# Optimization experiments

Hardware: AMD Instinct MI355X
Metric: run time of the kernel (lower is better)

The kernel has to match this reference:

```python
import jax, jax.numpy as jnp
import numpy as np

BN_EPS = 1e-5


def conv(x, w, b=None, stride=1, pad=1):
    out = jax.lax.conv_general_dilated(
        x, w, (stride, stride), [(pad, pad), (pad, pad)],
        dimension_numbers=("NCHW", "OIHW", "NCHW"))
    if b is not None:
        out = out + b[None, :, None, None]
    return out


def bn_relu(x):
    # BatchNorm2d(affine=False) in training mode: per-channel batch stats
    mean = jnp.mean(x, axis=(0, 2, 3), keepdims=True)
    var = jnp.var(x, axis=(0, 2, 3), keepdims=True)
    return jax.nn.relu((x - mean) * jax.lax.rsqrt(var + BN_EPS))


def deform_conv(x, offset, w, b, stride, pad=1):
    # torchvision DeformConv2d semantics, 3x3 kernel, dilation=1
    B, C, H, W = x.shape
    O = w.shape[0]
    K = 9
    Ho, Wo = offset.shape[2], offset.shape[3]
    off = offset.reshape(B, K, 2, Ho, Wo)  # (dy, dx) per kernel tap
    ky, kx = jnp.meshgrid(jnp.arange(3), jnp.arange(3), indexing="ij")
    ky = ky.reshape(K).astype(x.dtype)
    kx = kx.reshape(K).astype(x.dtype)
    oy = (jnp.arange(Ho) * stride - pad).astype(x.dtype)
    ox = (jnp.arange(Wo) * stride - pad).astype(x.dtype)
    # sampling coords [B,K,Ho,Wo]
    ys = oy[None, None, :, None] + ky[None, :, None, None] + off[:, :, 0]
    xs = ox[None, None, None, :] + kx[None, :, None, None] + off[:, :, 1]
    y0 = jnp.floor(ys)
    x0 = jnp.floor(xs)
    wy1 = ys - y0
    wx1 = xs - x0
    imf = x.reshape(B, C, H * W)

    def gather(iy, ix):
        valid = (iy >= 0) & (iy <= H - 1) & (ix >= 0) & (ix <= W - 1)
        iyc = jnp.clip(iy, 0, H - 1).astype(jnp.int32)
        ixc = jnp.clip(ix, 0, W - 1).astype(jnp.int32)
        lin = iyc * W + ixc  # [B,K,Ho,Wo]
        g = jax.vmap(lambda im, li: im[:, li])(imf, lin)  # [B,C,K,Ho,Wo]
        return g * valid[:, None].astype(x.dtype)

    sampled = (gather(y0, x0) * ((1 - wy1) * (1 - wx1))[:, None]
               + gather(y0, x0 + 1) * ((1 - wy1) * wx1)[:, None]
               + gather(y0 + 1, x0) * (wy1 * (1 - wx1))[:, None]
               + gather(y0 + 1, x0 + 1) * (wy1 * wx1)[:, None])
    out = jnp.einsum("ock,bckhw->bohw", w.reshape(O, C, K), sampled)
    return out + b[None, :, None, None]


def avgpool4(x):
    B, C, H, W = x.shape
    return x.reshape(B, C, H // 4, 4, W // 4, 4).mean(axis=(3, 5))


def setup_inputs() -> dict:
    key = jax.random.key(0)
    ks = jax.random.split(key, 20)
    n = jax.random.normal
    s = 0.05
    return {
        "x": n(ks[0], (8, 3, 640, 640), jnp.float32),
        "w_off1": n(ks[1], (18, 3, 3, 3), jnp.float32) * s,
        "b_off1": jnp.zeros((18,), jnp.float32),
        "w_d1": n(ks[2], (64, 3, 3, 3), jnp.float32) * s,
        "b_d1": jnp.zeros((64,), jnp.float32),
        "w_skip": n(ks[3], (64, 3, 1, 1), jnp.float32) * s,
        "b_skip": jnp.zeros((64,), jnp.float32),
        "w_bl1": n(ks[4], (64, 64, 3, 3), jnp.float32) * s,
        "w_bl2": n(ks[5], (64, 64, 3, 3), jnp.float32) * s,
        "w_off2": n(ks[6], (18, 64, 3, 3), jnp.float32) * s,
        "b_off2": jnp.zeros((18,), jnp.float32),
        "w_d2": n(ks[7], (64, 64, 3, 3), jnp.float32) * s,
        "b_d2": jnp.zeros((64,), jnp.float32),
        "w_off3": n(ks[8], (18, 64, 3, 3), jnp.float32) * s,
        "b_off3": jnp.zeros((18,), jnp.float32),
        "w_d3": n(ks[9], (256, 64, 3, 3), jnp.float32) * s,
        "b_d3": jnp.zeros((256,), jnp.float32),
    }


def reference(x, w_off1, b_off1, w_d1, b_d1, w_skip, b_skip, w_bl1, w_bl2,
              w_off2, b_off2, w_d2, b_d2, w_off3, b_off3, w_d3, b_d3):
    offset1 = conv(x, w_off1, b_off1, stride=4)
    d1 = deform_conv(x, offset1, w_d1, b_d1, stride=4)
    skip = conv(avgpool4(x), w_skip, b_skip, stride=1, pad=0)
    f = bn_relu(conv(d1 + skip, w_bl1))
    feat_1_4 = bn_relu(conv(f, w_bl2))
    offset2 = conv(feat_1_4, w_off2, b_off2, stride=2)
    feat_1_8 = deform_conv(feat_1_4, offset2, w_d2, b_d2, stride=2)
    offset3 = conv(feat_1_8, w_off3, b_off3, stride=2)
    feat_1_16 = deform_conv(feat_1_8, offset3, w_d3, b_d3, stride=2)
    return (feat_1_4, feat_1_8, feat_1_16)
```

## Files before the change

### kernel.cpp

```cpp
#include <hip/hip_runtime.h>
#include <hip/hip_bf16.h>
#include <math.h>

#define TPB 256

typedef __attribute__((ext_vector_type(8))) short bf16x8_t;
typedef __attribute__((ext_vector_type(4))) float f32x4_t;
typedef __attribute__((ext_vector_type(4))) int i32x4_t;
typedef __attribute__((ext_vector_type(4))) unsigned short u16x4_t;

static __device__ __forceinline__ float bf16_to_f(unsigned short s) {
    union { unsigned u; float f; } cv;
    cv.u = ((unsigned)s) << 16;
    return cv.f;
}
static __device__ __forceinline__ short f_to_bf16(float v) {
    __hip_bfloat16 h = __float2bfloat16(v);
    return *(short*)&h;
}

__global__ void repack_frag_kernel(const float* __restrict__ w,
                                   short* __restrict__ wtf,
                                   int Oreal, int NFRAG)
{
    int idx = blockIdx.x * TPB + threadIdx.x;
    int total = 18 * NFRAG * 64 * 8;
    if (idx >= total) return;
    int j    = idx & 7;
    int lane = (idx >> 3) & 63;
    int t    = idx >> 9;
    int ocf  = t % NFRAG;
    int kc   = t / NFRAG;
    int oc   = ocf * 16 + (lane & 15);
    int tap  = kc >> 1;
    int ic   = (kc & 1) * 32 + (lane >> 4) * 8 + j;
    float v = 0.f;
    if (oc < Oreal)
        v = w[((size_t)(oc * 64 + ic)) * 9 + tap];
    wtf[idx] = f_to_bf16(v);
}

__global__ void repack_d1_kernel(const float* __restrict__ w,
                                 short* __restrict__ wtf)
{
    int idx = blockIdx.x * TPB + threadIdx.x;
    if (idx >= 2048) return;
    int j    = idx & 7;
    int lane = (idx >> 3) & 63;
    int ocf  = idx >> 9;
    int oc   = ocf * 16 + (lane & 15);
    int k    = (lane >> 4) * 8 + j;
    float v = 0.f;
    if (k < 27) v = w[(size_t)oc * 27 + k];
    wtf[idx] = f_to_bf16(v);
}

template <int NORM>
__global__ __launch_bounds__(256, 2) void conv3x3_mfma_kernel(
    const short* __restrict__ xh,
    const short* __restrict__ wt,
    short* __restrict__ outh,
    float* __restrict__ stats,
    const float* __restrict__ stats_in,
    float invN,
    const float* __restrict__ zp)
{
    __shared__ short tile[2816 * 8];
    __shared__ float sstat[128];
    __shared__ float sm[64], sr[64];
    const int H = 160, W = 160, HW = 25600;
    int blk = blockIdx.x;
    int b  = blk / 100;
    int r  = blk % 100;
    int y0 = (r / 10) * 16;
    int x0 = (r % 10) * 16;
    const int tid = threadIdx.x;
    const short* inb = xh + (size_t)b * HW * 64;

    if (tid < 128) sstat[tid] = 0.f;
    if (NORM) {
        if (tid < 64) {
            float s = 0.f, s2 = 0.f;
#pragma unroll
            for (int k = 0; k < 8; ++k) {
                s  += stats_in[k * 128 + tid];
                s2 += stats_in[k * 128 + 64 + tid];
            }
            float mean = s * invN;
            float var  = s2 * invN - mean * mean;
            sm[tid] = mean;
            sr[tid] = rsqrtf(var + 1e-5f);
        }
        __syncthreads();
    }

#pragma unroll
    for (int it = 0; it < 11; ++it) {
        int item = it * 256 + tid;
        int c8  = item & 7;
        int pix = item >> 3;
        int row = pix / 18;
        int col = pix - row * 18;
        int y = y0 + row - 1;
        int x = x0 + col - 1;
        bool ok = (pix < 324) & (y >= 0) & (y < H) & (x >= 0) & (x < W);
        int cs = c8 ^ (col & 7);
        const short* src = ok
            ? &inb[((size_t)y * W + x) * 64 + (cs << 3)]
            : (const short*)zp;
        bf16x8_t v = *(const bf16x8_t*)src;
        if (NORM) {
            int cs8 = cs << 3;
            bf16x8_t o;
#pragma unroll
            for (int j = 0; j < 8; ++j) {
                float f = (bf16_to_f((unsigned short)v[j]) - sm[cs8 + j]) * sr[cs8 + j];
                f = f > 0.f ? f : 0.f;
                o[j] = ok ? f_to_bf16(f) : (short)0;
            }
            v = o;
        }
        *(bf16x8_t*)&tile[item * 8] = v;
    }
    __syncthreads();

    const int wv  = tid >> 6;
    const int l   = tid & 63;
    const int l15 = l & 15;
    const int lg  = l >> 4;

    f32x4_t acc[4][4];
#pragma unroll
    for (int i = 0; i < 4; ++i)
#pragma unroll
        for (int j = 0; j < 4; ++j)
            acc[i][j] = (f32x4_t){0.f, 0.f, 0.f, 0.f};

    bf16x8_t bfp[2][4], afp[2][4];
#pragma unroll
    for (int nf = 0; nf < 4; ++nf)
        bfp[0][nf] = *(const bf16x8_t*)(wt + (((size_t)(0 * 4 + nf)) * 64 + l) * 8);
    {
        int colr = l15;
        int chunk = lg ^ (colr & 7);
#pragma unroll
        for (int mf = 0; mf < 4; ++mf)
            afp[0][mf] = *(const bf16x8_t*)&tile[((wv * 4 + mf) * 18 + colr) * 64 + chunk * 8];
    }
#pragma unroll
    for (int kc = 0; kc < 18; ++kc) {
        const int cur = kc & 1, nxt = cur ^ 1;
        if (kc + 1 < 18) {
            int kn = kc + 1;
#pragma unroll
            for (int nf = 0; nf < 4; ++nf)
                bfp[nxt][nf] = *(const bf16x8_t*)(wt + (((size_t)(kn * 4 + nf)) * 64 + l) * 8);
            int tap = kn >> 1;
            int dy = tap / 3, dx = tap % 3;
            int colr = l15 + dx;
            int chunk = (((kn & 1) << 2) + lg) ^ (colr & 7);
#pragma unroll
            for (int mf = 0; mf < 4; ++mf)
                afp[nxt][mf] = *(const bf16x8_t*)&tile[((wv * 4 + mf + dy) * 18 + colr) * 64 + chunk * 8];
        }
#pragma unroll
        for (int mf = 0; mf < 4; ++mf)
#pragma unroll
            for (int nf = 0; nf < 4; ++nf)
                acc[mf][nf] = __builtin_amdgcn_mfma_f32_16x16x32_bf16(
                    afp[cur][mf], bfp[cur][nf], acc[mf][nf], 0, 0, 0);
    }

    __syncthreads();
#pragma unroll
    for (int mf = 0; mf < 4; ++mf) {
        int py = wv * 4 + mf;
#pragma unroll
        for (int nf = 0; nf < 4; ++nf) {
            int oc = nf * 16 + l15;
#pragma unroll
            for (int k = 0; k < 4; ++k)
                tile[((py * 16) + lg * 4 + k) * 64 + oc] = f_to_bf16(acc[mf][nf][k]);
        }
    }
    __syncthreads();
    short* outb = outh + (size_t)b * HW * 64;
#pragma unroll
    for (int j = 0; j < 8; ++j) {
        int item = j * 256 + tid;
        int c8  = item & 7;
        int pix = item >> 3;
        int py  = pix >> 4, px = pix & 15;
        *(bf16x8_t*)&outb[((size_t)(y0 + py) * W + x0 + px) * 64 + c8 * 8] =
            *(bf16x8_t*)&tile[pix * 64 + c8 * 8];
    }

#pragma unroll
    for (int nf = 0; nf < 4; ++nf) {
        float s = 0.f, s2 = 0.f;
#pragma unroll
        for (int mf = 0; mf < 4; ++mf)
#pragma unroll
            for (int k = 0; k < 4; ++k) {
                float v = acc[mf][nf][k];
                s += v; s2 += v * v;
            }
        s  += __shfl_xor(s, 16, 64);  s  += __shfl_xor(s, 32, 64);
        s2 += __shfl_xor(s2, 16, 64); s2 += __shfl_xor(s2, 32, 64);
        if (lg == 0) {
            int oc = nf * 16 + l15;
            atomicAdd(&sstat[oc], s);
            atomicAdd(&sstat[64 + oc], s2);
        }
    }
    __syncthreads();
    float* st = stats + (size_t)(blockIdx.x & 7) * 128;
    if (tid < 128) atomicAdd(&st[tid], sstat[tid]);
}

__global__ void nchw_to_nhwc_bf16_kernel(const float* __restrict__ in,
                                         short* __restrict__ out, int HW)
{
    __shared__ short tile[64][66];
    int nchunks = HW >> 6;
    int b  = blockIdx.x / nchunks;
    int p0 = (blockIdx.x % nchunks) << 6;
    int tid = threadIdx.x;
#pragma unroll
    for (int rep = 0; rep < 16; ++rep) {
        int item = rep * 256 + tid;
        int c = item >> 6, p = item & 63;
        tile[p][c] = f_to_bf16(in[((size_t)b * 64 + c) * HW + p0 + p]);
    }
    __syncthreads();
#pragma unroll
    for (int rep = 0; rep < 16; ++rep) {
        int item = rep * 256 + tid;
        int p = item >> 6, c = item & 63;
        out[((size_t)b * HW + p0 + p) * 64 + c] = tile[p][c];
    }
}

__global__ void bn_apply_dual_kernel(const short* __restrict__ in,
                                     const float* __restrict__ stats,
                                     float* __restrict__ out,
                                     short* __restrict__ outh,
                                     int HW, float invN)
{
    __shared__ float ftile[64][65];
    __shared__ float sm[64], sr[64];
    int nchunks = HW >> 6;
    int b  = blockIdx.x / nchunks;
    int p0 = (blockIdx.x % nchunks) << 6;
    int tid = threadIdx.x;
    if (tid < 64) {
        float s = 0.f, s2 = 0.f;
#pragma unroll
        for (int k = 0; k < 8; ++k) {
            s  += stats[k * 128 + tid];
            s2 += stats[k * 128 + 64 + tid];
        }
        float mean = s * invN;
        float var  = s2 * invN - mean * mean;
        sm[tid] = mean;
        sr[tid] = rsqrtf(var + 1e-5f);
    }
    __syncthreads();
#pragma unroll
    for (int it = 0; it < 2; ++it) {
        int item = it * 256 + tid;
        int p = item >> 3, c0 = (item & 7) * 8;
        size_t gi = ((size_t)(b * HW + p0 + p)) * 64 + c0;
        bf16x8_t v = *(const bf16x8_t*)&in[gi];
        bf16x8_t o;
#pragma unroll
        for (int j = 0; j < 8; ++j) {
            float f = (bf16_to_f((unsigned short)v[j]) - sm[c0 + j]) * sr[c0 + j];
            f = f > 0.f ? f : 0.f;
            ftile[p][c0 + j] = f;
            o[j] = f_to_bf16(f);
        }
        *(bf16x8_t*)&outh[gi] = o;
    }
    __syncthreads();
#pragma unroll
    for (int rep = 0; rep < 16; ++rep) {
        int item = rep * 256 + tid;
        int c = item >> 6, p = item & 63;
        out[((size_t)b * 64 + c) * HW + p0 + p] = ftile[p][c];
    }
}

__global__ void x_to_nhwc4_kernel(const float* __restrict__ in,
                                  float* __restrict__ out)
{
    int idx = blockIdx.x * TPB + threadIdx.x;
    const int HW = 640 * 640;
    if (idx >= 8 * HW) return;
    int b = idx / HW, p = idx % HW;
    f32x4_t v;
    v[0] = in[((size_t)b * 3 + 0) * HW + p];
    v[1] = in[((size_t)b * 3 + 1) * HW + p];
    v[2] = in[((size_t)b * 3 + 2) * HW + p];
    v[3] = 0.f;
    *(f32x4_t*)&out[(size_t)idx * 4] = v;
}

__global__ __launch_bounds__(256, 1) void offconv_mfma_kernel(
    const short* __restrict__ xh,
    const short* __restrict__ wt,
    const float* __restrict__ bias,
    float* __restrict__ out,
    int H, int W, int Ho, int Wo)
{
    const int HW = Ho * Wo;
    const int tid = threadIdx.x;
    const int wv = tid >> 6, l = tid & 63;
    const int l15 = l & 15, lg = l >> 4;
    const int pix0 = blockIdx.x * 64 + wv * 16;
    const int b = pix0 / HW;
    const int r0 = pix0 - b * HW;

    int rp = r0 + l15;
    int ho = rp / Wo, wo = rp % Wo;
    const short* xb = xh + (size_t)b * H * W * 64;

    f32x4_t acc[2];
    acc[0] = (f32x4_t){0.f, 0.f, 0.f, 0.f};
    acc[1] = (f32x4_t){0.f, 0.f, 0.f, 0.f};

#pragma unroll 2
    for (int kc = 0; kc < 18; ++kc) {
        int tap = kc >> 1;
        int iy = ho * 2 - 1 + tap / 3;
        int ix = wo * 2 - 1 + tap % 3;
        bf16x8_t af = {};
        if (iy >= 0 && iy < H && ix >= 0 && ix < W)
            af = *(const bf16x8_t*)&xb[((size_t)iy * W + ix) * 64
                                       + (kc & 1) * 32 + lg * 8];
#pragma unroll
        for (int nf = 0; nf < 2; ++nf) {
            bf16x8_t bf = *(const bf16x8_t*)(wt + (((size_t)(kc * 2 + nf)) * 64 + l) * 8);
            acc[nf] = __builtin_amdgcn_mfma_f32_16x16x32_bf16(af, bf, acc[nf], 0, 0, 0);
        }
    }

#pragma unroll
    for (int nf = 0; nf < 2; ++nf) {
        int oc = nf * 16 + l15;
        if (oc < 18) {
            float bv = bias[oc];
            f32x4_t v = acc[nf];
            v[0] += bv; v[1] += bv; v[2] += bv; v[3] += bv;
            *(f32x4_t*)&out[((size_t)(b * 18 + oc)) * HW + r0 + lg * 4] = v;
        }
    }
}

__global__ __launch_bounds__(256, 1) void deform1_kernel(
    const float* __restrict__ x4,
    const float* __restrict__ wof,
    const float* __restrict__ bof,
    const short* __restrict__ wtd1,
    const float* __restrict__ bias,
    const float* __restrict__ pool,
    const float* __restrict__ wsk,
    const float* __restrict__ bsk,
    short* __restrict__ outh)
{
    const int H = 640, W = 640, Ho = 160, Wo = 160, HW = 25600;
    constexpr int P = 32;
    __shared__ float xtap[P * 9][4];
    __shared__ float swof[486];
    __shared__ float sbof[18];
    __shared__ float spool[3][P];
    __shared__ float off1[P][18];
    __shared__ alignas(16) short sampb[P][40];
    __shared__ int   sidx[P * 9][4];
    __shared__ float swt[P * 9][4];
    const int tid = threadIdx.x;
    const int pix0 = blockIdx.x * P;
    const int b = pix0 / HW;
    const int r0 = pix0 - b * HW;
    const float* xb = x4 + (size_t)b * H * W * 4;

    for (int item = tid; item < P * 9; item += TPB) {
        int p = item / 9, tap = item % 9;
        int r = r0 + p, ho = r / Wo, wo = r % Wo;
        int iy = ho * 4 - 1 + tap / 3;
        int ix = wo * 4 - 1 + tap % 3;
        f32x4_t s = (f32x4_t){0.f, 0.f, 0.f, 0.f};
        if (iy >= 0 && iy < H && ix >= 0 && ix < W)
            s = *(const f32x4_t*)&xb[((size_t)iy * W + ix) * 4];
        *(f32x4_t*)xtap[item] = s;
    }
    for (int i = tid; i < P * 40; i += TPB) ((short*)sampb)[i] = 0;
    for (int i = tid; i < 96; i += TPB) {
        int c = i >> 5, p = i & 31;
        spool[c][p] = pool[((size_t)(b * 3 + c)) * HW + r0 + p];
    }
    for (int item = tid; item < 486; item += TPB) swof[item] = wof[item];
    if (tid < 18) sbof[tid] = bof[tid];
    __syncthreads();

    for (int item = tid; item < P * 18; item += TPB) {
        int p = item / 18, o = item % 18;
        float acc = sbof[o];
#pragma unroll
        for (int tap = 0; tap < 9; ++tap) {
            const float* xt = xtap[p * 9 + tap];
#pragma unroll
            for (int c = 0; c < 3; ++c)
                acc += xt[c] * swof[(o * 3 + c) * 9 + tap];
        }
        off1[p][o] = acc;
    }
    __syncthreads();

    for (int item = tid; item < P * 9; item += TPB) {
        int p = item / 9, tap = item % 9;
        int r = r0 + p, ho = r / Wo, wo = r % Wo;
        float dy = off1[p][2 * tap];
        float dx = off1[p][2 * tap + 1];
        float ys = (float)(ho * 4 - 1 + tap / 3) + dy;
        float xs = (float)(wo * 4 - 1 + tap % 3) + dx;
        float y0f = floorf(ys), x0f = floorf(xs);
        float fy = ys - y0f, fx = xs - x0f;
        int y0 = (int)y0f, x0 = (int)x0f;
        float wts[4] = {(1.f - fy) * (1.f - fx), (1.f - fy) * fx,
                        fy * (1.f - fx),          fy * fx};
#pragma unroll
        for (int j = 0; j < 4; ++j) {
            int iy = y0 + (j >> 1), ix = x0 + (j & 1);
            bool v = (iy >= 0) && (iy < H) && (ix >= 0) && (ix < W);
            sidx[item][j] = v ? (iy * W + ix) : 0;
            swt[item][j]  = v ? wts[j] : 0.f;
        }
    }
    __syncthreads();

    for (int item = tid; item < P * 9; item += TPB) {
        int p = item / 9, tap = item % 9;
        i32x4_t id4 = *(const i32x4_t*)sidx[item];
        f32x4_t w4  = *(const f32x4_t*)swt[item];
        f32x4_t a0 = *(const f32x4_t*)&xb[(size_t)(unsigned)id4[0] * 4];
        f32x4_t a1 = *(const f32x4_t*)&xb[(size_t)(unsigned)id4[1] * 4];
        f32x4_t a2 = *(const f32x4_t*)&xb[(size_t)(unsigned)id4[2] * 4];
        f32x4_t a3 = *(const f32x4_t*)&xb[(size_t)(unsigned)id4[3] * 4];
        sampb[p][0 * 9 + tap] = f_to_bf16(
            w4[0]*a0[0] + w4[1]*a1[0] + w4[2]*a2[0] + w4[3]*a3[0]);
        sampb[p][1 * 9 + tap] = f_to_bf16(
            w4[0]*a0[1] + w4[1]*a1[1] + w4[2]*a2[1] + w4[3]*a3[1]);
        sampb[p][2 * 9 + tap] = f_to_bf16(
            w4[0]*a0[2] + w4[1]*a1[2] + w4[2]*a2[2] + w4[3]*a3[2]);
    }
    __syncthreads();

    const int wv = tid >> 6;
    const int l  = tid & 63;
    const int l15 = l & 15, lg = l >> 4;
    bf16x8_t bf  = *(const bf16x8_t*)(wtd1 + (((size_t)wv * 64 + l)) * 8);
    bf16x8_t af0 = *(const bf16x8_t*)&sampb[l15][lg * 8];
    bf16x8_t af1 = *(const bf16x8_t*)&sampb[l15 + 16][lg * 8];
    f32x4_t z = (f32x4_t){0.f, 0.f, 0.f, 0.f};
    f32x4_t acc0 = __builtin_amdgcn_mfma_f32_16x16x32_bf16(af0, bf, z, 0, 0, 0);
    f32x4_t acc1 = __builtin_amdgcn_mfma_f32_16x16x32_bf16(af1, bf, z, 0, 0, 0);

    int oc = wv * 16 + l15;
    float bb = bias[oc] + bsk[oc];
    float w0 = wsk[oc * 3 + 0], w1 = wsk[oc * 3 + 1], w2 = wsk[oc * 3 + 2];
    short* otile = (short*)xtap;
    __syncthreads();
#pragma unroll
    for (int mf = 0; mf < 2; ++mf) {
        f32x4_t a = mf ? acc1 : acc0;
#pragma unroll
        for (int k = 0; k < 4; ++k) {
            int px = mf * 16 + lg * 4 + k;
            float sv = w0 * spool[0][px] + w1 * spool[1][px] + w2 * spool[2][px];
            otile[px * 64 + oc] = f_to_bf16(a[k] + bb + sv);
        }
    }
    __syncthreads();
    {
        int c8 = tid & 7, px = tid >> 3;
        *(bf16x8_t*)&outh[((size_t)(b * HW + r0 + px)) * 64 + c8 * 8] =
            *(bf16x8_t*)&otile[px * 64 + c8 * 8];
    }
}

template <int O>
__global__ __launch_bounds__(256, 1) void deform_mfma_kernel(
    const short* __restrict__ xh,
    const float* __restrict__ off,
    const short* __restrict__ wt,
    const float* __restrict__ bias,
    float* __restrict__ out,
    int H, int W, int Ho, int Wo, int stride)
{
    constexpr int NF = O / 64;
    constexpr int NFRAG = O / 16;
    constexpr int P  = 32;
    __shared__ alignas(16) short samp[P * 576];
    __shared__ int   sidx[P * 9][4];
    __shared__ float swt[P * 9][4];

    const int tid = threadIdx.x;
    const int HW = Ho * Wo;
    const int pix0 = blockIdx.x * P;
    const int b = pix0 / HW;
    const int r0 = pix0 - b * HW;

    for (int item = tid; item < P * 9; item += TPB) {
        int p = item / 9, tap = item % 9;
        int r = r0 + p, ho = r / Wo, wo = r % Wo;
        float dy = off[((size_t)(b * 18 + 2 * tap) * Ho + ho) * Wo + wo];
        float dx = off[((size_t)(b * 18 + 2 * tap + 1) * Ho + ho) * Wo + wo];
        float ys = (float)(ho * stride - 1 + tap / 3) + dy;
        float xs = (float)(wo * stride - 1 + tap % 3) + dx;
        float y0f = floorf(ys), x0f = floorf(xs);
        float fy = ys - y0f, fx = xs - x0f;
        int y0 = (int)y0f, x0 = (int)x0f;
        float wts[4] = {(1.f - fy) * (1.f - fx), (1.f - fy) * fx,
                        fy * (1.f - fx),          fy * fx};
#pragma unroll
        for (int j = 0; j < 4; ++j) {
            int iy = y0 + (j >> 1), ix = x0 + (j & 1);
            bool v = (iy >= 0) && (iy < H) && (ix >= 0) && (ix < W);
            sidx[item][j] = v ? (iy * W + ix) : 0;
            swt[item][j]  = v ? wts[j] : 0.f;
        }
    }
    __syncthreads();

    {
        const int grp = tid >> 4;
        const int ic  = (tid & 15) * 4;
        const short* xb = xh + (size_t)b * H * W * 64;
#pragma unroll 3
        for (int i = 0; i < 18; ++i) {
            int e = grp * 18 + i;
            int p = e / 9, tap = e % 9;
            i32x4_t id4 = *(const i32x4_t*)sidx[e];
            f32x4_t w4  = *(const f32x4_t*)swt[e];
            u16x4_t u0 = *(const u16x4_t*)&xb[(size_t)(unsigned)id4[0] * 64 + ic];
            u16x4_t u1 = *(const u16x4_t*)&xb[(size_t)(unsigned)id4[1] * 64 + ic];
            u16x4_t u2 = *(const u16x4_t*)&xb[(size_t)(unsigned)id4[2] * 64 + ic];
            u16x4_t u3 = *(const u16x4_t*)&xb[(size_t)(unsigned)id4[3] * 64 + ic];
            float v0 = w4[0]*bf16_to_f(u0[0]) + w4[1]*bf16_to_f(u1[0])
                     + w4[2]*bf16_to_f(u2[0]) + w4[3]*bf16_to_f(u3[0]);
            float v1 = w4[0]*bf16_to_f(u0[1]) + w4[1]*bf16_to_f(u1[1])
                     + w4[2]*bf16_to_f(u2[1]) + w4[3]*bf16_to_f(u3[1]);
            float v2 = w4[0]*bf16_to_f(u0[2]) + w4[1]*bf16_to_f(u1[2])
                     + w4[2]*bf16_to_f(u2[2]) + w4[3]*bf16_to_f(u3[2]);
            float v3 = w4[0]*bf16_to_f(u0[3]) + w4[1]*bf16_to_f(u1[3])
                     + w4[2]*bf16_to_f(u2[3]) + w4[3]*bf16_to_f(u3[3]);
            int sw = (tap * 8 + ((ic >> 3) ^ (p & 7))) * 8 + (ic & 7);
            short* dst = &samp[p * 576 + sw];
            dst[0] = f_to_bf16(v0);
            dst[1] = f_to_bf16(v1);
            dst[2] = f_to_bf16(v2);
            dst[3] = f_to_bf16(v3);
        }
    }
    __syncthreads();

    const int wv = tid >> 6;
    const int l  = tid & 63;
    const int l15 = l & 15, lg = l >> 4;
    f32x4_t acc[2][NF];
#pragma unroll
    for (int mf = 0; mf < 2; ++mf)
#pragma unroll
        for (int nf = 0; nf < NF; ++nf)
            acc[mf][nf] = (f32x4_t){0.f, 0.f, 0.f, 0.f};

#pragma unroll 2
    for (int kc = 0; kc < 18; ++kc) {
        int tap = kc >> 1;
        int low = (((kc & 1) << 2) | lg) ^ (l15 & 7);
        bf16x8_t af0 = *(const bf16x8_t*)&samp[l15 * 576 + (tap * 8 + low) * 8];
        bf16x8_t af1 = *(const bf16x8_t*)&samp[(l15 + 16) * 576 + (tap * 8 + low) * 8];
#pragma unroll
        for (int nf = 0; nf < NF; ++nf) {
            int ocf = wv * NF + nf;
            bf16x8_t bf = *(const bf16x8_t*)(wt + (((size_t)(kc * NFRAG + ocf)) * 64 + l) * 8);
            acc[0][nf] = __builtin_amdgcn_mfma_f32_16x16x32_bf16(af0, bf, acc[0][nf], 0, 0, 0);
            acc[1][nf] = __builtin_amdgcn_mfma_f32_16x16x32_bf16(af1, bf, acc[1][nf], 0, 0, 0);
        }
    }

#pragma unroll
    for (int mf = 0; mf < 2; ++mf)
#pragma unroll
        for (int nf = 0; nf < NF; ++nf) {
            int oc = (wv * NF + nf) * 16 + l15;
            float bv = bias[oc];
            f32x4_t v = acc[mf][nf];
            v[0] += bv; v[1] += bv; v[2] += bv; v[3] += bv;
            *(f32x4_t*)&out[((size_t)(b * O + oc)) * HW + r0 + mf * 16 + lg * 4] = v;
        }
}

__global__ void avgpool4_kernel(const float* __restrict__ in,
                                float* __restrict__ out,
                                int BC, int Ho, int Wo, int H, int W)
{
    int idx = blockIdx.x * TPB + threadIdx.x;
    int total = BC * Ho * Wo;
    if (idx >= total) return;
    int wo = idx % Wo;
    int t = idx / Wo;
    int ho = t % Ho;
    int bc = t / Ho;
    const float* xp = in + (size_t)bc * H * W + (ho * 4) * W + wo * 4;
    float s = 0.f;
#pragma unroll
    for (int i = 0; i < 4; ++i)
#pragma unroll
        for (int j = 0; j < 4; ++j)
            s += xp[i * W + j];
    out[idx] = s * (1.0f / 16.0f);
}

__global__ void zero_stats_kernel(float* __restrict__ stats)
{
    int i = threadIdx.x;
#pragma unroll
    for (int k = 0; k < 8; ++k) stats[k * 256 + i] = 0.f;
    stats[2048 + i] = 0.f;
    stats[2048 + 256 + i] = 0.f;
}

extern "C" void kernel_launch(void* const* d_in, const int* in_sizes, int n_in,
                              void* d_out, int out_size, void* d_ws, size_t ws_size,
                              hipStream_t stream)
{
    const float* x      = (const float*)d_in[0];
    const float* w_off1 = (const float*)d_in[1];
    const float* b_off1 = (const float*)d_in[2];
    const float* w_d1   = (const float*)d_in[3];
    const float* b_d1   = (const float*)d_in[4];
    const float* w_skip = (const float*)d_in[5];
    const float* b_skip = (const float*)d_in[6];
    const float* w_bl1  = (const float*)d_in[7];
    const float* w_bl2  = (const float*)d_in[8];
    const float* w_off2 = (const float*)d_in[9];
    const float* b_off2 = (const float*)d_in[10];
    const float* w_d2   = (const float*)d_in[11];
    const float* b_d2   = (const float*)d_in[12];
    const float* w_off3 = (const float*)d_in[13];
    const float* b_off3 = (const float*)d_in[14];
    const float* w_d3   = (const float*)d_in[15];
    const float* b_d3   = (const float*)d_in[16];

    const int B = 8;
    float* A     = (float*)d_ws;
    float* bufB  = A + 3686400;
    float* bufC  = bufB + 13107200;

    short* hB   = (short*)bufB;
    short* hC   = (short*)bufC;
    float* pool = bufB + 8000000;

    short* wt1    = (short*)(A + 1000000);
    short* wt2    = wt1 + 18 * 4 * 512;
    short* wtd2   = (short*)(A + 1500000);
    short* wtd3   = (short*)(A + 1550000);
    short* wtoff2 = (short*)(A + 1700000);
    short* wtoff3 = (short*)(A + 1712000);
    short* wtd1   = (short*)(A + 1750000);
    float* stats1 = A + 1800000;
    float* stats2 = stats1 + 1024;
    float* zpage  = stats1 + 2048;

    float* out0 = (float*)d_out;
    float* out1 = out0 + 13107200;
    float* out2 = out1 + 3276800;

    const float invN = 1.0f / (B * 25600);

    x_to_nhwc4_kernel<<<(8 * 409600 + TPB - 1) / TPB, TPB, 0, stream>>>(x, bufC);

    avgpool4_kernel<<<(B * 3 * 25600 + TPB - 1) / TPB, TPB, 0, stream>>>(
        x, pool, B * 3, 160, 160, 640, 640);

    repack_frag_kernel<<<(18 * 4 * 512 + TPB - 1) / TPB, TPB, 0, stream>>>(w_bl1, wt1, 64, 4);
    repack_frag_kernel<<<(18 * 4 * 512 + TPB - 1) / TPB, TPB, 0, stream>>>(w_bl2, wt2, 64, 4);
    repack_frag_kernel<<<(18 * 4 * 512 + TPB - 1) / TPB, TPB, 0, stream>>>(w_d2, wtd2, 64, 4);
    repack_frag_kernel<<<(18 * 16 * 512 + TPB - 1) / TPB, TPB, 0, stream>>>(w_d3, wtd3, 256, 16);
    repack_frag_kernel<<<(18 * 2 * 512 + TPB - 1) / TPB, TPB, 0, stream>>>(w_off2, wtoff2, 18, 2);
    repack_frag_kernel<<<(18 * 2 * 512 + TPB - 1) / TPB, TPB, 0, stream>>>(w_off3, wtoff3, 18, 2);
    repack_d1_kernel<<<8, TPB, 0, stream>>>(w_d1, wtd1);
    zero_stats_kernel<<<1, 256, 0, stream>>>(stats1);

    deform1_kernel<<<8 * 25600 / 32, TPB, 0, stream>>>(
        bufC, w_off1, b_off1, wtd1, b_d1, pool, w_skip, b_skip, hB);

    conv3x3_mfma_kernel<0><<<800, TPB, 0, stream>>>(
        hB, wt1, hC, stats1, nullptr, invN, zpage);

    conv3x3_mfma_kernel<1><<<800, TPB, 0, stream>>>(
        hC, wt2, hB, stats2, stats1, invN, zpage);

    bn_apply_dual_kernel<<<8 * 400, TPB, 0, stream>>>(
        hB, stats2, out0, hC, 25600, invN);

    offconv_mfma_kernel<<<8 * 6400 / 64, TPB, 0, stream>>>(
        hC, wtoff2, b_off2, A, 160, 160, 80, 80);

    deform_mfma_kernel<64><<<8 * 6400 / 32, TPB, 0, stream>>>(
        hC, A, wtd2, b_d2, out1, 160, 160, 80, 80, 2);

    nchw_to_nhwc_bf16_kernel<<<8 * (6400 / 64), TPB, 0, stream>>>(out1, hB, 6400);

    offconv_mfma_kernel<<<8 * 1600 / 64, TPB, 0, stream>>>(
        hB, wtoff3, b_off3, A, 80, 80, 40, 40);

    deform_mfma_kernel<256><<<8 * 1600 / 32, TPB, 0, stream>>>(
        hB, A, wtd3, b_d3, out2, 80, 80, 40, 40, 2);
}
```

Before: 238.0 us.

## Fuse input prep, weight repacks and NHWC conversion into fewer kernels

Merges the NCHW-to-NHWC4 conversion and the 4x4 average pool into a single prep kernel that reads the input once with vector loads. All weight repacks and the stats zeroing are folded into one launch. The deform conv at 1/8 scale now also writes its bf16 NHWC copy from the accumulators through shared memory, which removes the separate transpose kernel and its re-read of out1. The aim is fewer launches and less global traffic, at the cost of an extra shared-memory pass and sync in the deform kernel.

```diff
diff --git a/kernel.cpp b/kernel.cpp
--- a/kernel.cpp
+++ b/kernel.cpp
@@ -19,13 +19,42 @@
     return *(short*)&h;
 }
 
-__global__ void repack_frag_kernel(const float* __restrict__ w,
-                                   short* __restrict__ wtf,
-                                   int Oreal, int NFRAG)
-{
+__global__ void prep_kernel(const float* __restrict__ in,
+                            float* __restrict__ x4,
+                            float* __restrict__ pool)
+{
+    const int HWo = 25600, H = 640, W = 640;
     int idx = blockIdx.x * TPB + threadIdx.x;
-    int total = 18 * NFRAG * 64 * 8;
-    if (idx >= total) return;
+    if (idx >= 8 * HWo) return;
+    int b = idx / HWo, r = idx % HWo;
+    int ho = r / 160, wo = r % 160;
+    float s0 = 0.f, s1 = 0.f, s2 = 0.f;
+    float* x4b = x4 + (size_t)b * H * W * 4;
+#pragma unroll
+    for (int dy = 0; dy < 4; ++dy) {
+        int row = ho * 4 + dy;
+        size_t base = ((size_t)row * W + wo * 4);
+        f32x4_t a0 = *(const f32x4_t*)&in[((size_t)(b * 3 + 0) * H * W) + base];
+        f32x4_t a1 = *(const f32x4_t*)&in[((size_t)(b * 3 + 1) * H * W) + base];
+        f32x4_t a2 = *(const f32x4_t*)&in[((size_t)(b * 3 + 2) * H * W) + base];
+        s0 += a0[0] + a0[1] + a0[2] + a0[3];
+        s1 += a1[0] + a1[1] + a1[2] + a1[3];
+        s2 += a2[0] + a2[1] + a2[2] + a2[3];
+#pragma unroll
+        for (int dx = 0; dx < 4; ++dx) {
+            f32x4_t v = (f32x4_t){a0[dx], a1[dx], a2[dx], 0.f};
+            *(f32x4_t*)&x4b[(base + dx) * 4] = v;
+        }
+    }
+    pool[((size_t)(b * 3 + 0)) * HWo + r] = s0 * (1.0f / 16.0f);
+    pool[((size_t)(b * 3 + 1)) * HWo + r] = s1 * (1.0f / 16.0f);
+    pool[((size_t)(b * 3 + 2)) * HWo + r] = s2 * (1.0f / 16.0f);
+}
+
+static __device__ __forceinline__ void repack_one(
+    const float* __restrict__ w, short* __restrict__ wtf,
+    int idx, int Oreal, int NFRAG)
+{
     int j    = idx & 7;
     int lane = (idx >> 3) & 63;
     int t    = idx >> 9;
@@ -40,19 +69,40 @@
     wtf[idx] = f_to_bf16(v);
 }
 
-__global__ void repack_d1_kernel(const float* __restrict__ w,
-                                 short* __restrict__ wtf)
+__global__ void repack_all_kernel(
+    const float* __restrict__ w_bl1, short* __restrict__ wt1,
+    const float* __restrict__ w_bl2, short* __restrict__ wt2,
+    const float* __restrict__ w_d2,  short* __restrict__ wtd2,
+    const float* __restrict__ w_d3,  short* __restrict__ wtd3,
+    const float* __restrict__ w_off2, short* __restrict__ wtoff2,
+    const float* __restrict__ w_off3, short* __restrict__ wtoff3,
+    const float* __restrict__ w_d1,  short* __restrict__ wtd1,
+    float* __restrict__ stats)
 {
     int idx = blockIdx.x * TPB + threadIdx.x;
-    if (idx >= 2048) return;
-    int j    = idx & 7;
-    int lane = (idx >> 3) & 63;
-    int ocf  = idx >> 9;
-    int oc   = ocf * 16 + (lane & 15);
-    int k    = (lane >> 4) * 8 + j;
-    float v = 0.f;
-    if (k < 27) v = w[(size_t)oc * 27 + k];
-    wtf[idx] = f_to_bf16(v);
+    if (idx < 36864) { repack_one(w_bl1, wt1, idx, 64, 4); return; }
+    idx -= 36864;
+    if (idx < 36864) { repack_one(w_bl2, wt2, idx, 64, 4); return; }
+    idx -= 36864;
+    if (idx < 36864) { repack_one(w_d2, wtd2, idx, 64, 4); return; }
+    idx -= 36864;
+    if (idx < 147456) { repack_one(w_d3, wtd3, idx, 256, 16); return; }
+    idx -= 147456;
+    if (idx < 18432) { repack_one(w_off2, wtoff2, idx, 18, 2); return; }
+    idx -= 18432;
+    if (idx < 18432) { repack_one(w_off3, wtoff3, idx, 18, 2); return; }
+    idx -= 18432;
+    if (idx < 2048) {
+        int j = idx & 7, lane = (idx >> 3) & 63, ocf = idx >> 9;
+        int oc = ocf * 16 + (lane & 15);
+        int k  = (lane >> 4) * 8 + j;
+        float v = 0.f;
+        if (k < 27) v = w_d1[(size_t)oc * 27 + k];
+        wtd1[idx] = f_to_bf16(v);
+        return;
+    }
+    idx -= 2048;
+    if (idx < 2560) stats[idx] = 0.f;
 }
 
 template <int NORM>
@@ -218,29 +268,6 @@
     if (tid < 128) atomicAdd(&st[tid], sstat[tid]);
 }
 
-__global__ void nchw_to_nhwc_bf16_kernel(const float* __restrict__ in,
-                                         short* __restrict__ out, int HW)
-{
-    __shared__ short tile[64][66];
-    int nchunks = HW >> 6;
-    int b  = blockIdx.x / nchunks;
-    int p0 = (blockIdx.x % nchunks) << 6;
-    int tid = threadIdx.x;
-#pragma unroll
-    for (int rep = 0; rep < 16; ++rep) {
-        int item = rep * 256 + tid;
-        int c = item >> 6, p = item & 63;
-        tile[p][c] = f_to_bf16(in[((size_t)b * 64 + c) * HW + p0 + p]);
-    }
-    __syncthreads();
-#pragma unroll
-    for (int rep = 0; rep < 16; ++rep) {
-        int item = rep * 256 + tid;
-        int p = item >> 6, c = item & 63;
-        out[((size_t)b * HW + p0 + p) * 64 + c] = tile[p][c];
-    }
-}
-
 __global__ void bn_apply_dual_kernel(const short* __restrict__ in,
                                      const float* __restrict__ stats,
                                      float* __restrict__ out,
@@ -289,21 +316,6 @@
         int c = item >> 6, p = item & 63;
         out[((size_t)b * 64 + c) * HW + p0 + p] = ftile[p][c];
     }
-}
-
-__global__ void x_to_nhwc4_kernel(const float* __restrict__ in,
-                                  float* __restrict__ out)
-{
-    int idx = blockIdx.x * TPB + threadIdx.x;
-    const int HW = 640 * 640;
-    if (idx >= 8 * HW) return;
-    int b = idx / HW, p = idx % HW;
-    f32x4_t v;
-    v[0] = in[((size_t)b * 3 + 0) * HW + p];
-    v[1] = in[((size_t)b * 3 + 1) * HW + p];
-    v[2] = in[((size_t)b * 3 + 2) * HW + p];
-    v[3] = 0.f;
-    *(f32x4_t*)&out[(size_t)idx * 4] = v;
 }
 
 __global__ __launch_bounds__(256, 1) void offconv_mfma_kernel(
@@ -489,13 +501,14 @@
     }
 }
 
-template <int O>
+template <int O, int DUAL>
 __global__ __launch_bounds__(256, 1) void deform_mfma_kernel(
     const short* __restrict__ xh,
     const float* __restrict__ off,
     const short* __restrict__ wt,
     const float* __restrict__ bias,
     float* __restrict__ out,
+    short* __restrict__ outh,
     int H, int W, int Ho, int Wo, int stride)
 {
     constexpr int NF = O / 64;
@@ -598,38 +611,27 @@
             float bv = bias[oc];
             f32x4_t v = acc[mf][nf];
             v[0] += bv; v[1] += bv; v[2] += bv; v[3] += bv;
+            acc[mf][nf] = v;
             *(f32x4_t*)&out[((size_t)(b * O + oc)) * HW + r0 + mf * 16 + lg * 4] = v;
         }
-}
-
-__global__ void avgpool4_kernel(const float* __restrict__ in,
-                                float* __restrict__ out,
-                                int BC, int Ho, int Wo, int H, int W)
-{
-    int idx = blockIdx.x * TPB + threadIdx.x;
-    int total = BC * Ho * Wo;
-    if (idx >= total) return;
-    int wo = idx % Wo;
-    int t = idx / Wo;
-    int ho = t % Ho;
-    int bc = t / Ho;
-    const float* xp = in + (size_t)bc * H * W + (ho * 4) * W + wo * 4;
-    float s = 0.f;
-#pragma unroll
-    for (int i = 0; i < 4; ++i)
-#pragma unroll
-        for (int j = 0; j < 4; ++j)
-            s += xp[i * W + j];
-    out[idx] = s * (1.0f / 16.0f);
-}
-
-__global__ void zero_stats_kernel(float* __restrict__ stats)
-{
-    int i = threadIdx.x;
-#pragma unroll
-    for (int k = 0; k < 8; ++k) stats[k * 256 + i] = 0.f;
-    stats[2048 + i] = 0.f;
-    stats[2048 + 256 + i] = 0.f;
+
+    if (DUAL) {
+        __syncthreads();
+        short* otile = samp;
+#pragma unroll
+        for (int mf = 0; mf < 2; ++mf) {
+            int oc = wv * 16 + l15;
+#pragma unroll
+            for (int k = 0; k < 4; ++k) {
+                int px = mf * 16 + lg * 4 + k;
+                otile[px * 64 + oc] = f_to_bf16(acc[mf][0][k]);
+            }
+        }
+        __syncthreads();
+        int c8 = tid & 7, px = tid >> 3;
+        *(bf16x8_t*)&outh[((size_t)(b * HW + r0 + px)) * 64 + c8 * 8] =
+            *(bf16x8_t*)&otile[px * 64 + c8 * 8];
+    }
 }
 
 extern "C" void kernel_launch(void* const* d_in, const int* in_sizes, int n_in,
@@ -680,19 +682,11 @@
 
     const float invN = 1.0f / (B * 25600);
 
-    x_to_nhwc4_kernel<<<(8 * 409600 + TPB - 1) / TPB, TPB, 0, stream>>>(x, bufC);
-
-    avgpool4_kernel<<<(B * 3 * 25600 + TPB - 1) / TPB, TPB, 0, stream>>>(
-        x, pool, B * 3, 160, 160, 640, 640);
-
-    repack_frag_kernel<<<(18 * 4 * 512 + TPB - 1) / TPB, TPB, 0, stream>>>(w_bl1, wt1, 64, 4);
-    repack_frag_kernel<<<(18 * 4 * 512 + TPB - 1) / TPB, TPB, 0, stream>>>(w_bl2, wt2, 64, 4);
-    repack_frag_kernel<<<(18 * 4 * 512 + TPB - 1) / TPB, TPB, 0, stream>>>(w_d2, wtd2, 64, 4);
-    repack_frag_kernel<<<(18 * 16 * 512 + TPB - 1) / TPB, TPB, 0, stream>>>(w_d3, wtd3, 256, 16);
-    repack_frag_kernel<<<(18 * 2 * 512 + TPB - 1) / TPB, TPB, 0, stream>>>(w_off2, wtoff2, 18, 2);
-    repack_frag_kernel<<<(18 * 2 * 512 + TPB - 1) / TPB, TPB, 0, stream>>>(w_off3, wtoff3, 18, 2);
-    repack_d1_kernel<<<8, TPB, 0, stream>>>(w_d1, wtd1);
-    zero_stats_kernel<<<1, 256, 0, stream>>>(stats1);
+    prep_kernel<<<(8 * 25600 + TPB - 1) / TPB, TPB, 0, stream>>>(x, bufC, pool);
+
+    repack_all_kernel<<<(299520 + TPB - 1) / TPB, TPB, 0, stream>>>(
+        w_bl1, wt1, w_bl2, wt2, w_d2, wtd2, w_d3, wtd3,
+        w_off2, wtoff2, w_off3, wtoff3, w_d1, wtd1, stats1);
 
     deform1_kernel<<<8 * 25600 / 32, TPB, 0, stream>>>(
         bufC, w_off1, b_off1, wtd1, b_d1, pool, w_skip, b_skip, hB);
@@ -709,14 +703,12 @@
     offconv_mfma_kernel<<<8 * 6400 / 64, TPB, 0, stream>>>(
         hC, wtoff2, b_off2, A, 160, 160, 80, 80);
 
-    deform_mfma_kernel<64><<<8 * 6400 / 32, TPB, 0, stream>>>(
-        hC, A, wtd2, b_d2, out1, 160, 160, 80, 80, 2);
-
-    nchw_to_nhwc_bf16_kernel<<<8 * (6400 / 64), TPB, 0, stream>>>(out1, hB, 6400);
+    deform_mfma_kernel<64, 1><<<8 * 6400 / 32, TPB, 0, stream>>>(
+        hC, A, wtd2, b_d2, out1, hB, 160, 160, 80, 80, 2);
 
     offconv_mfma_kernel<<<8 * 1600 / 64, TPB, 0, stream>>>(
         hB, wtoff3, b_off3, A, 80, 80, 40, 40);
 
-    deform_mfma_kernel<256><<<8 * 1600 / 32, TPB, 0, stream>>>(
-        hB, A, wtd3, b_d3, out2, 80, 80, 40, 40, 2);
-}
+    deform_mfma_kernel<256, 0><<<8 * 1600 / 32, TPB, 0, stream>>>(
+        hB, A, wtd3, b_d3, out2, nullptr, 80, 80, 40, 40, 2);
+}
```

After: 224.7 us. 1.06x faster.
